# Kernel tuning notes

Hardware: AMD Instinct MI355X
Metric: run time of the kernel (lower is better)

## Reference

```python
import jax, jax.numpy as jnp
import numpy as np

B, S, HID, H, RELC = 2, 1024, 1024, 16, 64
D = HID // H          # head dim = 64
R = 2 * RELC + 1      # 129 relative-position buckets
NEG_INF = -10000.0
LN_EPS = 1e-12


def setup_inputs() -> dict:
    key = jax.random.key(0)
    ks = jax.random.split(key, 16)
    s = 0.02
    return {
        "query": jax.random.normal(ks[0], (B, S, HID), jnp.float32),
        "key": jax.random.normal(ks[1], (B, S, HID), jnp.float32),
        "value": jax.random.normal(ks[2], (B, S, HID), jnp.float32),
        "mask_k": jnp.ones((B, S), jnp.float32),
        "mask_qk": jnp.ones((B, S, S), jnp.float32),
        "rposi": jax.random.randint(ks[3], (B, S, S), 0, R, jnp.int32),
        "Wq": jax.random.normal(ks[4], (HID, HID), jnp.float32) * s,
        "bq": jnp.zeros((HID,), jnp.float32),
        "Wk": jax.random.normal(ks[5], (HID, HID), jnp.float32) * s,
        "bk": jnp.zeros((HID,), jnp.float32),
        "Wv": jax.random.normal(ks[6], (HID, HID), jnp.float32) * s,
        "bv": jnp.zeros((HID,), jnp.float32),
        "Wd": jax.random.normal(ks[7], (HID, HID), jnp.float32) * s,
        "bd": jnp.zeros((HID,), jnp.float32),
        "ln_g": jnp.ones((HID,), jnp.float32),
        "ln_b": jnp.zeros((HID,), jnp.float32),
        "edge_atts": jax.random.normal(ks[8], (R, D), jnp.float32) * s,
        "edge_values": jax.random.normal(ks[9], (R, D), jnp.float32) * s,
    }


def _heads(x):  # [B,S,HID] -> [B,H,S,D]
    return x.reshape(B, -1, H, D).transpose(0, 2, 1, 3)


def reference(query, key, value, mask_k, mask_qk, rposi,
              Wq, bq, Wk, bk, Wv, bv, Wd, bd, ln_g, ln_b,
              edge_atts, edge_values):
    q = _heads(query @ Wq + bq)   # [B,H,Q,D]
    k = _heads(key @ Wk + bk)     # [B,H,K,D]
    v = _heads(value @ Wv + bv)   # [B,H,K,D]

    rp = jnp.clip(rposi, -RELC, RELC) + RELC          # [B,Q,K] in [0,2*RELC]

    scores = jnp.einsum('bhqd,bhkd->bhqk', q, k)      # [B,H,Q,K]
    # relative-position attention bias: q . edge_atts[rp]
    q2 = jnp.einsum('bhqd,rd->bhqr', q, edge_atts)    # [B,H,Q,R]
    rscore = jnp.take_along_axis(
        q2, jnp.broadcast_to(rp[:, None], (B, H, S, S)), axis=-1)
    scores = (scores + rscore) / jnp.sqrt(jnp.float32(D))

    att_mask = mask_k[:, None, :] * mask_qk           # [B,Q,K]
    scores = scores + (1.0 - att_mask)[:, None] * NEG_INF
    probs = jax.nn.softmax(scores, axis=-1)           # [B,H,Q,K]

    ctx = jnp.einsum('bhqk,bhkd->bhqd', probs, v)     # [B,H,Q,D]
    rval = edge_values[rp]                            # [B,Q,K,D]
    ctx = ctx + jnp.einsum('bhqk,bqkd->bhqd', probs, rval)

    ctx = ctx.transpose(0, 2, 1, 3).reshape(B, S, HID)
    h = ctx @ Wd + bd
    x = h + query
    mu = jnp.mean(x, axis=-1, keepdims=True)
    var = jnp.mean(jnp.square(x - mu), axis=-1, keepdims=True)
    return (x - mu) * jax.lax.rsqrt(var + LN_EPS) * ln_g + ln_b
```

## Files before the change

kernel.cpp:

```cpp
#include <hip/hip_runtime.h>
#include <hip/hip_bf16.h>
#include <stdint.h>

#define B_    2
#define S_    1024
#define HID_  1024
#define H_    16
#define D_    64
#define R_    129
#define EST_  136
#define SENT_ 132
#define NTOK_ 2048
#define C2_   0.18033688011112042f

typedef __attribute__((ext_vector_type(8))) short bf16x8;
typedef __attribute__((ext_vector_type(4))) float f32x4;

__device__ __forceinline__ float bf2f(unsigned short s) {
  union { float f; unsigned int u; } v; v.u = ((unsigned int)s) << 16; return v.f;
}
__device__ __forceinline__ unsigned short f2bf(float f) {
  union { float f; unsigned int u; } v; v.f = f;
  return (unsigned short)((v.u + 0x7fff + ((v.u >> 16) & 1)) >> 16);
}

__global__ __launch_bounds__(256) void wt4_kernel(const float* __restrict__ Wq,
                                                  const float* __restrict__ Wk,
                                                  const float* __restrict__ Wv,
                                                  const float* __restrict__ Wd,
                                                  unsigned short* __restrict__ WqT,
                                                  unsigned short* __restrict__ WkT,
                                                  unsigned short* __restrict__ WvT,
                                                  unsigned short* __restrict__ WdT) {
  const float* W; unsigned short* Wt;
  switch (blockIdx.z) {
    case 0: W = Wq; Wt = WqT; break;
    case 1: W = Wk; Wt = WkT; break;
    case 2: W = Wv; Wt = WvT; break;
    default: W = Wd; Wt = WdT; break;
  }
  __shared__ float tile[32][33];
  const int n0 = blockIdx.x * 32, k0 = blockIdx.y * 32;
  const int tx = threadIdx.x, ty = threadIdx.y;
  #pragma unroll
  for (int i = 0; i < 32; i += 8)
    tile[ty + i][tx] = W[(size_t)(k0 + ty + i) * HID_ + n0 + tx];
  __syncthreads();
  #pragma unroll
  for (int i = 0; i < 32; i += 8)
    Wt[(size_t)(n0 + ty + i) * HID_ + k0 + tx] = f2bf(tile[tx][ty + i]);
}

__global__ __launch_bounds__(256) void evt_kernel(const float* __restrict__ EV,
                                                  unsigned short* __restrict__ EVt) {
  const int idx = blockIdx.x * 256 + threadIdx.x;
  if (idx < 64 * 160) {
    const int d = idx / 160, r = idx % 160;
    EVt[idx] = f2bf(r < R_ ? EV[(size_t)r * D_ + d] : 0.f);
  }
}

__global__ __launch_bounds__(256) void rpx_kernel(const int* __restrict__ rposi,
                                                  const float* __restrict__ mask_k,
                                                  const float* __restrict__ mask_qk,
                                                  unsigned char* __restrict__ rpx) {
  const int t = threadIdx.x;
  const int lo = t & 15, hi = (t >> 4) & 3, wq = (t >> 6) & 1, wk = (t >> 7) & 1;
  const int kt = blockIdx.x, q5 = blockIdx.y, b = blockIdx.z;
  unsigned char out[8];
  #pragma unroll
  for (int e = 0; e < 8; e++) {
    const int ct2 = e >> 2, j = e & 3;
    const int q = q5 * 32 + wq * 16 + hi * 4 + j;
    const int k = kt * 64 + wk * 32 + ct2 * 16 + lo;
    int rp = rposi[((size_t)b * S_ + q) * S_ + k];
    rp = min(max(rp, -64), 64) + 64;
    const float m = mask_qk[((size_t)b * S_ + q) * S_ + k] * mask_k[(size_t)b * S_ + k];
    out[e] = (m > 0.5f) ? (unsigned char)rp : (unsigned char)SENT_;
  }
  const size_t off = ((((((size_t)b * 32 + q5) * 16 + kt) * 2 + wk) * 2 + wq) * 4 + hi) * 16 + lo;
  *(uint2*)(rpx + off * 8) = *(uint2*)out;
}

__global__ __launch_bounds__(256) void qkv_gemm_kernel(
    const float* __restrict__ query, const float* __restrict__ key, const float* __restrict__ value,
    const unsigned short* __restrict__ WqT, const unsigned short* __restrict__ WkT,
    const unsigned short* __restrict__ WvT,
    const float* __restrict__ bq, const float* __restrict__ bk, const float* __restrict__ bvv,
    unsigned short* __restrict__ Qh, unsigned short* __restrict__ Kh, unsigned short* __restrict__ Vt) {
  const float* A; const unsigned short* Bt; const float* bias; unsigned short* Out; int omode;
  if (blockIdx.z == 0)      { A = query; Bt = WqT; bias = bq;  Out = Qh; omode = 0; }
  else if (blockIdx.z == 1) { A = key;   Bt = WkT; bias = bk;  Out = Kh; omode = 0; }
  else                      { A = value; Bt = WvT; bias = bvv; Out = Vt; omode = 1; }
  __shared__ __align__(16) unsigned short Alds[64][40];
  __shared__ __align__(16) unsigned short Blds[64][40];
  const int m0 = blockIdx.x * 64, n0 = blockIdx.y * 64;
  const int t = threadIdx.x;
  const int wave = t >> 6, lane = t & 63, lo = lane & 15, hi = lane >> 4;
  const int wr = wave >> 1, wc = wave & 1;
  const int row = t >> 2, col = (t & 3) * 8;
  const f32x4 zero4 = {0.f, 0.f, 0.f, 0.f};
  f32x4 acc[2][2] = {{zero4, zero4}, {zero4, zero4}};

  for (int k0 = 0; k0 < HID_; k0 += 32) {
    const float* asrc = A + (size_t)(m0 + row) * HID_ + k0 + col;
    f32x4 v0 = *(const f32x4*)asrc, v1 = *(const f32x4*)(asrc + 4);
    unsigned short ab[8];
    ab[0]=f2bf(v0.x); ab[1]=f2bf(v0.y); ab[2]=f2bf(v0.z); ab[3]=f2bf(v0.w);
    ab[4]=f2bf(v1.x); ab[5]=f2bf(v1.y); ab[6]=f2bf(v1.z); ab[7]=f2bf(v1.w);
    bf16x8 bb = *(const bf16x8*)(Bt + (size_t)(n0 + row) * HID_ + k0 + col);
    __syncthreads();
    *(bf16x8*)&Alds[row][col] = *(bf16x8*)ab;
    *(bf16x8*)&Blds[row][col] = bb;
    __syncthreads();
    bf16x8 af[2], bfr[2];
    #pragma unroll
    for (int a = 0; a < 2; a++) af[a]  = *(const bf16x8*)&Alds[wr*32 + a*16 + lo][hi*8];
    #pragma unroll
    for (int b2 = 0; b2 < 2; b2++) bfr[b2] = *(const bf16x8*)&Blds[wc*32 + b2*16 + lo][hi*8];
    #pragma unroll
    for (int a = 0; a < 2; a++)
      #pragma unroll
      for (int b2 = 0; b2 < 2; b2++)
        acc[a][b2] = __builtin_amdgcn_mfma_f32_16x16x32_bf16(af[a], bfr[b2], acc[a][b2], 0, 0, 0);
  }

  #pragma unroll
  for (int a = 0; a < 2; a++) {
    const int mg = m0 + wr*32 + a*16 + hi*4;
    #pragma unroll
    for (int b2 = 0; b2 < 2; b2++) {
      const int n = n0 + wc*32 + b2*16 + lo;
      const float bv = bias[n];
      const int hh = n >> 6, d = n & (D_ - 1);
      #pragma unroll
      for (int j = 0; j < 4; j++) {
        const float val = acc[a][b2][j] + bv;
        const int m = mg + j;
        const int bb = m >> 10, s = m & (S_ - 1);
        if (omode == 0)
          Out[(((size_t)(bb * H_ + hh)) * S_ + s) * D_ + d] = f2bf(val);
        else
          Out[(((size_t)(bb * H_ + hh)) * D_ + d) * S_ + s] = f2bf(val);
      }
    }
  }
}

__global__ __launch_bounds__(256) void d_gemm_kernel(const unsigned short* __restrict__ Actx,
                                                     const unsigned short* __restrict__ Bt,
                                                     const float* __restrict__ bias,
                                                     float* __restrict__ Out) {
  __shared__ __align__(16) unsigned short Alds[64][40];
  __shared__ __align__(16) unsigned short Blds[64][40];
  const int m0 = blockIdx.x * 64, n0 = blockIdx.y * 64;
  const int t = threadIdx.x;
  const int wave = t >> 6, lane = t & 63, lo = lane & 15, hi = lane >> 4;
  const int wr = wave >> 1, wc = wave & 1;
  const int row = t >> 2, col = (t & 3) * 8;
  const f32x4 zero4 = {0.f, 0.f, 0.f, 0.f};
  f32x4 acc[2][2] = {{zero4, zero4}, {zero4, zero4}};

  for (int k0 = 0; k0 < HID_; k0 += 32) {
    bf16x8 aa = *(const bf16x8*)(Actx + (size_t)(m0 + row) * HID_ + k0 + col);
    bf16x8 bb = *(const bf16x8*)(Bt + (size_t)(n0 + row) * HID_ + k0 + col);
    __syncthreads();
    *(bf16x8*)&Alds[row][col] = aa;
    *(bf16x8*)&Blds[row][col] = bb;
    __syncthreads();
    bf16x8 af[2], bfr[2];
    #pragma unroll
    for (int a = 0; a < 2; a++) af[a]  = *(const bf16x8*)&Alds[wr*32 + a*16 + lo][hi*8];
    #pragma unroll
    for (int b2 = 0; b2 < 2; b2++) bfr[b2] = *(const bf16x8*)&Blds[wc*32 + b2*16 + lo][hi*8];
    #pragma unroll
    for (int a = 0; a < 2; a++)
      #pragma unroll
      for (int b2 = 0; b2 < 2; b2++)
        acc[a][b2] = __builtin_amdgcn_mfma_f32_16x16x32_bf16(af[a], bfr[b2], acc[a][b2], 0, 0, 0);
  }

  #pragma unroll
  for (int a = 0; a < 2; a++) {
    const int mg = m0 + wr*32 + a*16 + hi*4;
    #pragma unroll
    for (int b2 = 0; b2 < 2; b2++) {
      const int n = n0 + wc*32 + b2*16 + lo;
      const float bv = bias[n];
      #pragma unroll
      for (int j = 0; j < 4; j++)
        Out[(size_t)(mg + j) * HID_ + n] = acc[a][b2][j] + bv;
    }
  }
}

__global__ __launch_bounds__(256) void eb_kernel(const unsigned short* __restrict__ Qh,
                                                 const float* __restrict__ EA,
                                                 unsigned short* __restrict__ Eb) {
  __shared__ __align__(16) unsigned short Qt[64][72];
  __shared__ __align__(16) unsigned short EAt[144][72];
  const int bh = blockIdx.y, s0 = blockIdx.x * 64;
  const int t = threadIdx.x, wave = t >> 6, lane = t & 63;
  const int lo = lane & 15, hi = lane >> 4;
  { const int row = t >> 2, c0 = (t & 3) * 16;
    const unsigned short* src = Qh + ((size_t)bh * S_ + s0 + row) * D_ + c0;
    *(bf16x8*)&Qt[row][c0]   = *(const bf16x8*)src;
    *(bf16x8*)&Qt[row][c0+8] = *(const bf16x8*)(src + 8); }
  for (int i = t; i < 144 * 64; i += 256) {
    const int r = i >> 6, d = i & 63;
    EAt[r][d] = f2bf(r < R_ ? EA[(size_t)r * D_ + d] : 0.f);
  }
  __syncthreads();
  bf16x8 af[2];
  af[0] = *(const bf16x8*)&Qt[wave*16 + lo][hi*8];
  af[1] = *(const bf16x8*)&Qt[wave*16 + lo][32 + hi*8];
  const f32x4 zero4 = {0.f, 0.f, 0.f, 0.f};
  f32x4 acc[9];
  #pragma unroll
  for (int rt = 0; rt < 9; rt++) acc[rt] = zero4;
  #pragma unroll
  for (int rt = 0; rt < 9; rt++)
    #pragma unroll
    for (int kk = 0; kk < 2; kk++) {
      bf16x8 bfr = *(const bf16x8*)&EAt[rt*16 + lo][kk*32 + hi*8];
      acc[rt] = __builtin_amdgcn_mfma_f32_16x16x32_bf16(af[kk], bfr, acc[rt], 0, 0, 0);
    }
  #pragma unroll
  for (int rt = 0; rt < 9; rt++) {
    const int r = rt * 16 + lo;
    if (r < EST_) {
      #pragma unroll
      for (int j = 0; j < 4; j++) {
        const int q = s0 + wave*16 + hi*4 + j;
        const float val = (r < R_) ? exp2f(acc[rt][j] * C2_) : 0.f;
        Eb[((size_t)bh * S_ + q) * EST_ + r] = f2bf(val);
      }
    }
  }
}


#define ABODY(KT, RX) do {                                                               \
    const int kw = (KT) * 64 + wk * 32;                                                  \
    int rpv[8];                                                                          \
    rpv[0] = (RX).x & 255;         rpv[1] = ((RX).x >> 8) & 255;                         \
    rpv[2] = ((RX).x >> 16) & 255; rpv[3] = (RX).x >> 24;                                \
    rpv[4] = (RX).y & 255;         rpv[5] = ((RX).y >> 8) & 255;                         \
    rpv[6] = ((RX).y >> 16) & 255; rpv[7] = (RX).y >> 24;                                \
    float ge[8];                                                                         \
    _Pragma("unroll")                                                                    \
    for (int e = 0; e < 8; e++)                                                          \
      ge[e] = bf2f(Uq.El[wq * 16 + hi * 4 + (e & 3)][rpv[e]]);                           \
    f32x4 sc0 = zero4, sc1 = zero4;                                                      \
    __builtin_amdgcn_s_setprio(1);                                                       \
    { bf16x8 kf0 = *(const bf16x8*)(Kbase + (size_t)(kw + lo) * D_ + hi * 8);            \
      bf16x8 kf1 = *(const bf16x8*)(Kbase + (size_t)(kw + lo) * D_ + 32 + hi * 8);       \
      bf16x8 kf2 = *(const bf16x8*)(Kbase + (size_t)(kw + 16 + lo) * D_ + hi * 8);       \
      bf16x8 kf3 = *(const bf16x8*)(Kbase + (size_t)(kw + 16 + lo) * D_ + 32 + hi * 8);  \
      sc0 = __builtin_amdgcn_mfma_f32_16x16x32_bf16(qfrag0, kf0, sc0, 0, 0, 0);          \
      sc0 = __builtin_amdgcn_mfma_f32_16x16x32_bf16(qfrag1, kf1, sc0, 0, 0, 0);          \
      sc1 = __builtin_amdgcn_mfma_f32_16x16x32_bf16(qfrag0, kf2, sc1, 0, 0, 0);          \
      sc1 = __builtin_amdgcn_mfma_f32_16x16x32_bf16(qfrag1, kf3, sc1, 0, 0, 0); }        \
    __builtin_amdgcn_s_setprio(0);                                                       \
    bf16x8 vf0 = *(const bf16x8*)(Vbase + (size_t)(lo) * S_ + kw + hi * 8);              \
    bf16x8 vf1 = *(const bf16x8*)(Vbase + (size_t)(16 + lo) * S_ + kw + hi * 8);         \
    bf16x8 vf2 = *(const bf16x8*)(Vbase + (size_t)(32 + lo) * S_ + kw + hi * 8);         \
    bf16x8 vf3 = *(const bf16x8*)(Vbase + (size_t)(48 + lo) * S_ + kw + hi * 8);         \
    _Pragma("unroll")                                                                    \
    for (int e = 0; e < 8; e++) {                                                        \
      const int j = e & 3;                                                               \
      const float sv = (e < 4) ? sc0[j] : sc1[j];                                        \
      const float p = exp2f(sv * C2_) * ge[e];                                           \
      lsum[j] += p;                                                                      \
      const int qr = wq * 16 + hi * 4 + j;                                               \
      if (rpv[e] == 128) r128[j] += p;                                                   \
      else atomicAdd(&hist[qr][rpv[e]], p);                                              \
      Plds[wave][hi * 4 + j][(e >> 2) * 16 + lo] = f2bf(p);                              \
    }                                                                                    \
    bf16x8 pf = *(const bf16x8*)&Plds[wave][lo][hi * 8];                                 \
    __builtin_amdgcn_s_setprio(1);                                                       \
    ctx[0] = __builtin_amdgcn_mfma_f32_16x16x32_bf16(pf, vf0, ctx[0], 0, 0, 0);          \
    ctx[1] = __builtin_amdgcn_mfma_f32_16x16x32_bf16(pf, vf1, ctx[1], 0, 0, 0);          \
    ctx[2] = __builtin_amdgcn_mfma_f32_16x16x32_bf16(pf, vf2, ctx[2], 0, 0, 0);          \
    ctx[3] = __builtin_amdgcn_mfma_f32_16x16x32_bf16(pf, vf3, ctx[3], 0, 0, 0);          \
    __builtin_amdgcn_s_setprio(0);                                                       \
  } while (0)

__global__ __launch_bounds__(256, 4) void attn_kernel(const unsigned short* __restrict__ Qh,
                                                      const unsigned short* __restrict__ Kh,
                                                      const unsigned short* __restrict__ Vt,
                                                      const unsigned short* __restrict__ Eb,
                                                      const unsigned char* __restrict__ rpx,
                                                      const unsigned short* __restrict__ EVt,
                                                      unsigned short* __restrict__ ctxb) {
  __shared__ union UU {
    unsigned short El[32][EST_];
    float red[2][16][65];
  } Uq;
  __shared__ float hist[32][EST_];
  __shared__ __align__(16) unsigned short Plds[4][16][40];
  __shared__ float lsumLDS[2][32];

  const int bh = blockIdx.y, b = bh >> 4, h = bh & 15;
  const int q5 = blockIdx.x, q0 = q5 * 32;
  const int t = threadIdx.x, wave = t >> 6, lane = t & 63;
  const int lo = lane & 15, hi = lane >> 4;
  const int wq = wave >> 1, wk = wave & 1;

  { const unsigned int* src = (const unsigned int*)(Eb + ((size_t)bh * S_ + q0) * EST_);
    unsigned int* dst = (unsigned int*)&Uq.El[0][0];
    for (int i = t; i < 32 * EST_ / 2; i += 256) dst[i] = src[i]; }
  for (int i = t; i < 32 * EST_; i += 256) (&hist[0][0])[i] = 0.f;

  bf16x8 qfrag0, qfrag1;
  { const unsigned short* qrow = Qh + ((size_t)bh * S_ + q0 + wq * 16 + lo) * D_;
    qfrag0 = *(const bf16x8*)(qrow + hi * 8);
    qfrag1 = *(const bf16x8*)(qrow + 32 + hi * 8); }

  const f32x4 zero4 = {0.f, 0.f, 0.f, 0.f};
  f32x4 ctx[4] = {zero4, zero4, zero4, zero4};
  float lsum[4] = {0.f, 0.f, 0.f, 0.f};
  float r128[4] = {0.f, 0.f, 0.f, 0.f};

  const unsigned short* Kbase = Kh + (size_t)bh * S_ * D_;
  const unsigned short* Vbase = Vt + (size_t)bh * D_ * S_;
  const unsigned char* RXp = rpx +
      (((((((size_t)b * 32 + q5) * 16) * 2 + wk) * 2 + wq) * 4 + hi) * 16 + lo) * 8;

  __syncthreads();

  uint2 rxA = *(const uint2*)(RXp);
  #pragma unroll 1
  for (int kt2 = 0; kt2 < 8; kt2++) {
    uint2 rxB = *(const uint2*)(RXp + (size_t)(2 * kt2 + 1) * 2048);
    ABODY(2 * kt2, rxA);
    if (kt2 < 7) rxA = *(const uint2*)(RXp + (size_t)(2 * kt2 + 2) * 2048);
    ABODY(2 * kt2 + 1, rxB);
  }

  #pragma unroll
  for (int j = 0; j < 4; j++) {
    float v = r128[j];
    v += __shfl_xor(v, 1); v += __shfl_xor(v, 2); v += __shfl_xor(v, 4); v += __shfl_xor(v, 8);
    if (lo == 0) atomicAdd(&hist[wq * 16 + hi * 4 + j][128], v);
    float w = lsum[j];
    w += __shfl_xor(w, 1); w += __shfl_xor(w, 2); w += __shfl_xor(w, 4); w += __shfl_xor(w, 8);
    if (lo == 0) lsumLDS[wk][wq * 16 + hi * 4 + j] = w;
  }
  __syncthreads();

  #pragma unroll
  for (int g2 = 0; g2 < 2; g2++) {
    const int r0 = (wk * 2 + g2) * 32;
    const float* hrow = &hist[wq * 16 + lo][r0 + hi * 8];
    bf16x8 hf;
    #pragma unroll
    for (int u = 0; u < 8; u++) hf[u] = (short)f2bf(hrow[u]);
    #pragma unroll
    for (int dt = 0; dt < 4; dt++) {
      bf16x8 ef = *(const bf16x8*)(EVt + (size_t)(dt * 16 + lo) * 160 + r0 + hi * 8);
      ctx[dt] = __builtin_amdgcn_mfma_f32_16x16x32_bf16(hf, ef, ctx[dt], 0, 0, 0);
    }
  }
  if (wk == 1) {
    #pragma unroll
    for (int dt = 0; dt < 4; dt++) {
      const float ev = bf2f(EVt[(size_t)(dt * 16 + lo) * 160 + 128]);
      #pragma unroll
      for (int j = 0; j < 4; j++) {
        ctx[dt][j] += hist[wq * 16 + hi * 4 + j][128] * ev;
        Uq.red[wq][hi * 4 + j][dt * 16 + lo] = ctx[dt][j];
      }
    }
  }
  __syncthreads();
  if (wk == 0) {
    float ls[4];
    #pragma unroll
    for (int j = 0; j < 4; j++)
      ls[j] = lsumLDS[0][wq * 16 + hi * 4 + j] + lsumLDS[1][wq * 16 + hi * 4 + j];
    #pragma unroll
    for (int dt = 0; dt < 4; dt++)
      #pragma unroll
      for (int j = 0; j < 4; j++) {
        const float val = (ctx[dt][j] + Uq.red[wq][hi * 4 + j][dt * 16 + lo]) / ls[j];
        const int q = q0 + wq * 16 + hi * 4 + j;
        ctxb[((size_t)b * S_ + q) * HID_ + h * D_ + dt * 16 + lo] = f2bf(val);
      }
  }
}

__global__ __launch_bounds__(256) void ln_kernel(const float* __restrict__ hbuf,
                                                 const float* __restrict__ query,
                                                 const float* __restrict__ g,
                                                 const float* __restrict__ bta,
                                                 float* __restrict__ out) {
  const int row = blockIdx.x, t = threadIdx.x;
  f32x4 hv = *(const f32x4*)(hbuf + (size_t)row * HID_ + t * 4);
  f32x4 qv = *(const f32x4*)(query + (size_t)row * HID_ + t * 4);
  f32x4 x;
  x.x = hv.x + qv.x; x.y = hv.y + qv.y; x.z = hv.z + qv.z; x.w = hv.w + qv.w;
  float s  = x.x + x.y + x.z + x.w;
  float s2 = x.x*x.x + x.y*x.y + x.z*x.z + x.w*x.w;
  #pragma unroll
  for (int m = 1; m < 64; m <<= 1) { s += __shfl_xor(s, m); s2 += __shfl_xor(s2, m); }
  __shared__ float w1[4], w2[4];
  const int wave = t >> 6;
  if ((t & 63) == 0) { w1[wave] = s; w2[wave] = s2; }
  __syncthreads();
  s  = w1[0] + w1[1] + w1[2] + w1[3];
  s2 = w2[0] + w2[1] + w2[2] + w2[3];
  const float mu  = s * (1.f / HID_);
  const float var = s2 * (1.f / HID_) - mu * mu;
  const float rstd = rsqrtf(var + 1e-12f);
  f32x4 gv = *(const f32x4*)(g + t * 4);
  f32x4 bv = *(const f32x4*)(bta + t * 4);
  f32x4 o;
  o.x = (x.x - mu) * rstd * gv.x + bv.x;
  o.y = (x.y - mu) * rstd * gv.y + bv.y;
  o.z = (x.z - mu) * rstd * gv.z + bv.z;
  o.w = (x.w - mu) * rstd * gv.w + bv.w;
  *(f32x4*)(out + (size_t)row * HID_ + t * 4) = o;
}

extern "C" void kernel_launch(void* const* d_in, const int* in_sizes, int n_in,
                              void* d_out, int out_size, void* d_ws, size_t ws_size,
                              hipStream_t stream) {
  const float* query   = (const float*)d_in[0];
  const float* key     = (const float*)d_in[1];
  const float* value   = (const float*)d_in[2];
  const float* mask_k  = (const float*)d_in[3];
  const float* mask_qk = (const float*)d_in[4];
  const int*   rposi   = (const int*)d_in[5];
  const float* Wq = (const float*)d_in[6];
  const float* bq = (const float*)d_in[7];
  const float* Wk = (const float*)d_in[8];
  const float* bk = (const float*)d_in[9];
  const float* Wv = (const float*)d_in[10];
  const float* bv = (const float*)d_in[11];
  const float* Wd = (const float*)d_in[12];
  const float* bd = (const float*)d_in[13];
  const float* ln_g = (const float*)d_in[14];
  const float* ln_b = (const float*)d_in[15];
  const float* edge_atts   = (const float*)d_in[16];
  const float* edge_values = (const float*)d_in[17];

  char* ws = (char*)d_ws;
  unsigned short* WqT  = (unsigned short*)(ws + 0);
  unsigned short* WkT  = (unsigned short*)(ws + 2097152);
  unsigned short* WvT  = (unsigned short*)(ws + 4194304);
  unsigned short* WdT  = (unsigned short*)(ws + 6291456);
  unsigned short* ctxb = (unsigned short*)(ws + 0);
  unsigned short* Qh   = (unsigned short*)(ws + 8388608);
  unsigned short* Kh   = (unsigned short*)(ws + 12582912);
  unsigned short* Vt   = (unsigned short*)(ws + 16777216);
  float*          hbuf = (float*)        (ws + 8388608);
  unsigned short* Eb   = (unsigned short*)(ws + 20971520);
  unsigned short* EVt  = (unsigned short*)(ws + 29884416);
  unsigned char*  rpx  = (unsigned char*) (ws + 29904896);

  wt4_kernel<<<dim3(32, 32, 4), dim3(32, 8), 0, stream>>>(Wq, Wk, Wv, Wd, WqT, WkT, WvT, WdT);
  evt_kernel<<<40, 256, 0, stream>>>(edge_values, EVt);
  rpx_kernel<<<dim3(16, 32, 2), 256, 0, stream>>>(rposi, mask_k, mask_qk, rpx);

  qkv_gemm_kernel<<<dim3(32, 16, 3), 256, 0, stream>>>(query, key, value, WqT, WkT, WvT,
                                                       bq, bk, bv, Qh, Kh, Vt);

  eb_kernel<<<dim3(S_/64, B_*H_), 256, 0, stream>>>(Qh, edge_atts, Eb);

  attn_kernel<<<dim3(S_/32, B_*H_), 256, 0, stream>>>(Qh, Kh, Vt, Eb, rpx, EVt, ctxb);

  d_gemm_kernel<<<dim3(32, 16), 256, 0, stream>>>(ctxb, WdT, bd, hbuf);

  ln_kernel<<<NTOK_, 256, 0, stream>>>(hbuf, query, ln_g, ln_b, (float*)d_out);
}
```

Baseline: 192.0 us.

## Use 128x128 GEMM tiles and defer relative-position histogram atomics past PV MFMA

The QKV and output-projection GEMMs now share a templated 128x128 tile body in which each wave computes 4x4 MFMA fragments. This raises data reuse per LDS load but leaves far fewer blocks: 384 for QKV and only 128 for the dense projection, which may underfill the GPU. In the attention kernel, the LDS atomic histogram updates and the r128 accumulation move to after the PV MFMAs, using bf16-rounded probabilities packed into registers, so the atomics can overlap the matrix work. That rounding slightly changes the numerics of the edge-value accumulation.

Result: slower. 209.4 us (+9.0%).

```diff
diff --git a/kernel.cpp b/kernel.cpp
--- a/kernel.cpp
+++ b/kernel.cpp
@@ -82,7 +82,86 @@
   *(uint2*)(rpx + off * 8) = *(uint2*)out;
 }
 
-__global__ __launch_bounds__(256) void qkv_gemm_kernel(
+template<int AMODE>
+__device__ __forceinline__ void gemm128_body(const void* __restrict__ Aptr,
+                                             const unsigned short* __restrict__ Bt,
+                                             const float* __restrict__ bias,
+                                             void* __restrict__ Out, int omode,
+                                             int m0, int n0) {
+  __shared__ __align__(16) unsigned short Alds[128][40];
+  __shared__ __align__(16) unsigned short Blds[128][40];
+  const int t = threadIdx.x;
+  const int wave = t >> 6, lane = t & 63, lo = lane & 15, hi = lane >> 4;
+  const int wr = wave >> 1, wc = wave & 1;
+  const int row = t >> 1, cb = (t & 1) * 16;
+  const f32x4 zero4 = {0.f, 0.f, 0.f, 0.f};
+  f32x4 acc[4][4];
+  #pragma unroll
+  for (int a = 0; a < 4; a++)
+    #pragma unroll
+    for (int b = 0; b < 4; b++) acc[a][b] = zero4;
+
+  for (int k0 = 0; k0 < HID_; k0 += 32) {
+    unsigned short abuf[16];
+    if (AMODE == 0) {
+      const float* s = (const float*)Aptr + (size_t)(m0 + row) * HID_ + k0 + cb;
+      f32x4 v0 = *(const f32x4*)s, v1 = *(const f32x4*)(s + 4);
+      f32x4 v2 = *(const f32x4*)(s + 8), v3 = *(const f32x4*)(s + 12);
+      abuf[0]=f2bf(v0.x); abuf[1]=f2bf(v0.y); abuf[2]=f2bf(v0.z); abuf[3]=f2bf(v0.w);
+      abuf[4]=f2bf(v1.x); abuf[5]=f2bf(v1.y); abuf[6]=f2bf(v1.z); abuf[7]=f2bf(v1.w);
+      abuf[8]=f2bf(v2.x); abuf[9]=f2bf(v2.y); abuf[10]=f2bf(v2.z); abuf[11]=f2bf(v2.w);
+      abuf[12]=f2bf(v3.x); abuf[13]=f2bf(v3.y); abuf[14]=f2bf(v3.z); abuf[15]=f2bf(v3.w);
+    } else {
+      const unsigned short* s = (const unsigned short*)Aptr + (size_t)(m0 + row) * HID_ + k0 + cb;
+      *(bf16x8*)&abuf[0] = *(const bf16x8*)s;
+      *(bf16x8*)&abuf[8] = *(const bf16x8*)(s + 8);
+    }
+    bf16x8 bb0 = *(const bf16x8*)(Bt + (size_t)(n0 + row) * HID_ + k0 + cb);
+    bf16x8 bb1 = *(const bf16x8*)(Bt + (size_t)(n0 + row) * HID_ + k0 + cb + 8);
+    __syncthreads();
+    *(bf16x8*)&Alds[row][cb]     = *(bf16x8*)&abuf[0];
+    *(bf16x8*)&Alds[row][cb + 8] = *(bf16x8*)&abuf[8];
+    *(bf16x8*)&Blds[row][cb]     = bb0;
+    *(bf16x8*)&Blds[row][cb + 8] = bb1;
+    __syncthreads();
+    bf16x8 af[4], bfr[4];
+    #pragma unroll
+    for (int a = 0; a < 4; a++) af[a]  = *(const bf16x8*)&Alds[wr*64 + a*16 + lo][hi*8];
+    #pragma unroll
+    for (int b = 0; b < 4; b++) bfr[b] = *(const bf16x8*)&Blds[wc*64 + b*16 + lo][hi*8];
+    #pragma unroll
+    for (int a = 0; a < 4; a++)
+      #pragma unroll
+      for (int b = 0; b < 4; b++)
+        acc[a][b] = __builtin_amdgcn_mfma_f32_16x16x32_bf16(af[a], bfr[b], acc[a][b], 0, 0, 0);
+  }
+
+  #pragma unroll
+  for (int a = 0; a < 4; a++) {
+    const int mg = m0 + wr*64 + a*16 + hi*4;
+    #pragma unroll
+    for (int b = 0; b < 4; b++) {
+      const int n = n0 + wc*64 + b*16 + lo;
+      const float bv = bias[n];
+      #pragma unroll
+      for (int j = 0; j < 4; j++) {
+        const float val = acc[a][b][j] + bv;
+        const int m = mg + j;
+        if (omode == 2) {
+          ((float*)Out)[(size_t)m * HID_ + n] = val;
+        } else {
+          const int bb = m >> 10, s = m & (S_ - 1), hh = n >> 6, d = n & (D_ - 1);
+          if (omode == 0)
+            ((unsigned short*)Out)[(((size_t)(bb * H_ + hh)) * S_ + s) * D_ + d] = f2bf(val);
+          else
+            ((unsigned short*)Out)[(((size_t)(bb * H_ + hh)) * D_ + d) * S_ + s] = f2bf(val);
+        }
+      }
+    }
+  }
+}
+
+__global__ __launch_bounds__(256) void qkv_gemm128_kernel(
     const float* __restrict__ query, const float* __restrict__ key, const float* __restrict__ value,
     const unsigned short* __restrict__ WqT, const unsigned short* __restrict__ WkT,
     const unsigned short* __restrict__ WvT,
@@ -92,106 +171,14 @@
   if (blockIdx.z == 0)      { A = query; Bt = WqT; bias = bq;  Out = Qh; omode = 0; }
   else if (blockIdx.z == 1) { A = key;   Bt = WkT; bias = bk;  Out = Kh; omode = 0; }
   else                      { A = value; Bt = WvT; bias = bvv; Out = Vt; omode = 1; }
-  __shared__ __align__(16) unsigned short Alds[64][40];
-  __shared__ __align__(16) unsigned short Blds[64][40];
-  const int m0 = blockIdx.x * 64, n0 = blockIdx.y * 64;
-  const int t = threadIdx.x;
-  const int wave = t >> 6, lane = t & 63, lo = lane & 15, hi = lane >> 4;
-  const int wr = wave >> 1, wc = wave & 1;
-  const int row = t >> 2, col = (t & 3) * 8;
-  const f32x4 zero4 = {0.f, 0.f, 0.f, 0.f};
-  f32x4 acc[2][2] = {{zero4, zero4}, {zero4, zero4}};
-
-  for (int k0 = 0; k0 < HID_; k0 += 32) {
-    const float* asrc = A + (size_t)(m0 + row) * HID_ + k0 + col;
-    f32x4 v0 = *(const f32x4*)asrc, v1 = *(const f32x4*)(asrc + 4);
-    unsigned short ab[8];
-    ab[0]=f2bf(v0.x); ab[1]=f2bf(v0.y); ab[2]=f2bf(v0.z); ab[3]=f2bf(v0.w);
-    ab[4]=f2bf(v1.x); ab[5]=f2bf(v1.y); ab[6]=f2bf(v1.z); ab[7]=f2bf(v1.w);
-    bf16x8 bb = *(const bf16x8*)(Bt + (size_t)(n0 + row) * HID_ + k0 + col);
-    __syncthreads();
-    *(bf16x8*)&Alds[row][col] = *(bf16x8*)ab;
-    *(bf16x8*)&Blds[row][col] = bb;
-    __syncthreads();
-    bf16x8 af[2], bfr[2];
-    #pragma unroll
-    for (int a = 0; a < 2; a++) af[a]  = *(const bf16x8*)&Alds[wr*32 + a*16 + lo][hi*8];
-    #pragma unroll
-    for (int b2 = 0; b2 < 2; b2++) bfr[b2] = *(const bf16x8*)&Blds[wc*32 + b2*16 + lo][hi*8];
-    #pragma unroll
-    for (int a = 0; a < 2; a++)
-      #pragma unroll
-      for (int b2 = 0; b2 < 2; b2++)
-        acc[a][b2] = __builtin_amdgcn_mfma_f32_16x16x32_bf16(af[a], bfr[b2], acc[a][b2], 0, 0, 0);
-  }
-
-  #pragma unroll
-  for (int a = 0; a < 2; a++) {
-    const int mg = m0 + wr*32 + a*16 + hi*4;
-    #pragma unroll
-    for (int b2 = 0; b2 < 2; b2++) {
-      const int n = n0 + wc*32 + b2*16 + lo;
-      const float bv = bias[n];
-      const int hh = n >> 6, d = n & (D_ - 1);
-      #pragma unroll
-      for (int j = 0; j < 4; j++) {
-        const float val = acc[a][b2][j] + bv;
-        const int m = mg + j;
-        const int bb = m >> 10, s = m & (S_ - 1);
-        if (omode == 0)
-          Out[(((size_t)(bb * H_ + hh)) * S_ + s) * D_ + d] = f2bf(val);
-        else
-          Out[(((size_t)(bb * H_ + hh)) * D_ + d) * S_ + s] = f2bf(val);
-      }
-    }
-  }
-}
-
-__global__ __launch_bounds__(256) void d_gemm_kernel(const unsigned short* __restrict__ Actx,
-                                                     const unsigned short* __restrict__ Bt,
-                                                     const float* __restrict__ bias,
-                                                     float* __restrict__ Out) {
-  __shared__ __align__(16) unsigned short Alds[64][40];
-  __shared__ __align__(16) unsigned short Blds[64][40];
-  const int m0 = blockIdx.x * 64, n0 = blockIdx.y * 64;
-  const int t = threadIdx.x;
-  const int wave = t >> 6, lane = t & 63, lo = lane & 15, hi = lane >> 4;
-  const int wr = wave >> 1, wc = wave & 1;
-  const int row = t >> 2, col = (t & 3) * 8;
-  const f32x4 zero4 = {0.f, 0.f, 0.f, 0.f};
-  f32x4 acc[2][2] = {{zero4, zero4}, {zero4, zero4}};
-
-  for (int k0 = 0; k0 < HID_; k0 += 32) {
-    bf16x8 aa = *(const bf16x8*)(Actx + (size_t)(m0 + row) * HID_ + k0 + col);
-    bf16x8 bb = *(const bf16x8*)(Bt + (size_t)(n0 + row) * HID_ + k0 + col);
-    __syncthreads();
-    *(bf16x8*)&Alds[row][col] = aa;
-    *(bf16x8*)&Blds[row][col] = bb;
-    __syncthreads();
-    bf16x8 af[2], bfr[2];
-    #pragma unroll
-    for (int a = 0; a < 2; a++) af[a]  = *(const bf16x8*)&Alds[wr*32 + a*16 + lo][hi*8];
-    #pragma unroll
-    for (int b2 = 0; b2 < 2; b2++) bfr[b2] = *(const bf16x8*)&Blds[wc*32 + b2*16 + lo][hi*8];
-    #pragma unroll
-    for (int a = 0; a < 2; a++)
-      #pragma unroll
-      for (int b2 = 0; b2 < 2; b2++)
-        acc[a][b2] = __builtin_amdgcn_mfma_f32_16x16x32_bf16(af[a], bfr[b2], acc[a][b2], 0, 0, 0);
-  }
-
-  #pragma unroll
-  for (int a = 0; a < 2; a++) {
-    const int mg = m0 + wr*32 + a*16 + hi*4;
-    #pragma unroll
-    for (int b2 = 0; b2 < 2; b2++) {
-      const int n = n0 + wc*32 + b2*16 + lo;
-      const float bv = bias[n];
-      #pragma unroll
-      for (int j = 0; j < 4; j++)
-        Out[(size_t)(mg + j) * HID_ + n] = acc[a][b2][j] + bv;
-    }
-  }
+  gemm128_body<0>(A, Bt, bias, Out, omode, blockIdx.x * 128, blockIdx.y * 128);
+}
+
+__global__ __launch_bounds__(256) void d_gemm128_kernel(const unsigned short* __restrict__ Actx,
+                                                        const unsigned short* __restrict__ Bt,
+                                                        const float* __restrict__ bias,
+                                                        float* __restrict__ Out) {
+  gemm128_body<1>(Actx, Bt, bias, Out, 2, blockIdx.x * 128, blockIdx.y * 128);
 }
 
 __global__ __launch_bounds__(256) void eb_kernel(const unsigned short* __restrict__ Qh,
@@ -242,15 +229,12 @@
 
 #define ABODY(KT, RX) do {                                                               \
     const int kw = (KT) * 64 + wk * 32;                                                  \
-    int rpv[8];                                                                          \
-    rpv[0] = (RX).x & 255;         rpv[1] = ((RX).x >> 8) & 255;                         \
-    rpv[2] = ((RX).x >> 16) & 255; rpv[3] = (RX).x >> 24;                                \
-    rpv[4] = (RX).y & 255;         rpv[5] = ((RX).y >> 8) & 255;                         \
-    rpv[6] = ((RX).y >> 16) & 255; rpv[7] = (RX).y >> 24;                                \
     float ge[8];                                                                         \
     _Pragma("unroll")                                                                    \
-    for (int e = 0; e < 8; e++)                                                          \
-      ge[e] = bf2f(Uq.El[wq * 16 + hi * 4 + (e & 3)][rpv[e]]);                           \
+    for (int e = 0; e < 8; e++) {                                                        \
+      const int rp = (int)(((e < 4 ? (RX).x : (RX).y) >> ((e & 3) * 8)) & 255u);         \
+      ge[e] = bf2f(Uq.El[wq * 16 + hi * 4 + (e & 3)][rp]);                               \
+    }                                                                                    \
     f32x4 sc0 = zero4, sc1 = zero4;                                                      \
     __builtin_amdgcn_s_setprio(1);                                                       \
     { bf16x8 kf0 = *(const bf16x8*)(Kbase + (size_t)(kw + lo) * D_ + hi * 8);            \
@@ -266,16 +250,19 @@
     bf16x8 vf1 = *(const bf16x8*)(Vbase + (size_t)(16 + lo) * S_ + kw + hi * 8);         \
     bf16x8 vf2 = *(const bf16x8*)(Vbase + (size_t)(32 + lo) * S_ + kw + hi * 8);         \
     bf16x8 vf3 = *(const bf16x8*)(Vbase + (size_t)(48 + lo) * S_ + kw + hi * 8);         \
+    unsigned int pvp0, pvp1, pvp2, pvp3;                                                 \
     _Pragma("unroll")                                                                    \
     for (int e = 0; e < 8; e++) {                                                        \
       const int j = e & 3;                                                               \
       const float sv = (e < 4) ? sc0[j] : sc1[j];                                        \
       const float p = exp2f(sv * C2_) * ge[e];                                           \
       lsum[j] += p;                                                                      \
-      const int qr = wq * 16 + hi * 4 + j;                                               \
-      if (rpv[e] == 128) r128[j] += p;                                                   \
-      else atomicAdd(&hist[qr][rpv[e]], p);                                              \
-      Plds[wave][hi * 4 + j][(e >> 2) * 16 + lo] = f2bf(p);                              \
+      const unsigned int pb = f2bf(p);                                                   \
+      if (e == 0) pvp0 = pb;       else if (e == 1) pvp0 |= pb << 16;                    \
+      else if (e == 2) pvp1 = pb;  else if (e == 3) pvp1 |= pb << 16;                    \
+      else if (e == 4) pvp2 = pb;  else if (e == 5) pvp2 |= pb << 16;                    \
+      else if (e == 6) pvp3 = pb;  else              pvp3 |= pb << 16;                   \
+      Plds[wave][hi * 4 + j][(e >> 2) * 16 + lo] = (unsigned short)pb;                   \
     }                                                                                    \
     bf16x8 pf = *(const bf16x8*)&Plds[wave][lo][hi * 8];                                 \
     __builtin_amdgcn_s_setprio(1);                                                       \
@@ -284,6 +271,14 @@
     ctx[2] = __builtin_amdgcn_mfma_f32_16x16x32_bf16(pf, vf2, ctx[2], 0, 0, 0);          \
     ctx[3] = __builtin_amdgcn_mfma_f32_16x16x32_bf16(pf, vf3, ctx[3], 0, 0, 0);          \
     __builtin_amdgcn_s_setprio(0);                                                       \
+    _Pragma("unroll")                                                                    \
+    for (int e = 0; e < 8; e++) {                                                        \
+      const int rp = (int)(((e < 4 ? (RX).x : (RX).y) >> ((e & 3) * 8)) & 255u);         \
+      const unsigned int pw = (e < 2) ? pvp0 : (e < 4) ? pvp1 : (e < 6) ? pvp2 : pvp3;   \
+      const float pr = bf2f((unsigned short)((pw >> ((e & 1) * 16)) & 0xFFFFu));         \
+      if (rp == 128) r128[e & 3] += pr;                                                  \
+      else atomicAdd(&hist[wq * 16 + hi * 4 + (e & 3)][rp], pr);                         \
+    }                                                                                    \
   } while (0)
 
 __global__ __launch_bounds__(256, 4) void attn_kernel(const unsigned short* __restrict__ Qh,
@@ -463,14 +458,14 @@
   evt_kernel<<<40, 256, 0, stream>>>(edge_values, EVt);
   rpx_kernel<<<dim3(16, 32, 2), 256, 0, stream>>>(rposi, mask_k, mask_qk, rpx);
 
-  qkv_gemm_kernel<<<dim3(32, 16, 3), 256, 0, stream>>>(query, key, value, WqT, WkT, WvT,
-                                                       bq, bk, bv, Qh, Kh, Vt);
+  qkv_gemm128_kernel<<<dim3(16, 8, 3), 256, 0, stream>>>(query, key, value, WqT, WkT, WvT,
+                                                         bq, bk, bv, Qh, Kh, Vt);
 
   eb_kernel<<<dim3(S_/64, B_*H_), 256, 0, stream>>>(Qh, edge_atts, Eb);
 
   attn_kernel<<<dim3(S_/32, B_*H_), 256, 0, stream>>>(Qh, Kh, Vt, Eb, rpx, EVt, ctxb);
 
-  d_gemm_kernel<<<dim3(32, 16), 256, 0, stream>>>(ctxb, WdT, bd, hbuf);
+  d_gemm128_kernel<<<dim3(16, 8), 256, 0, stream>>>(ctxb, WdT, bd, hbuf);
 
   ln_kernel<<<NTOK_, 256, 0, stream>>>(hbuf, query, ln_g, ln_b, (float*)d_out);
 }
```

## Hoist K/V loads, defer histogram atomics past PV MFMA, remap attention block order

Applied to the files above, without the earlier changes.

The attention loop body now issues all K and V fragment loads before the QK MFMAs and moves the LDS histogram atomics after the PV MFMAs, using packed bf16 probabilities kept in registers. The goal is to overlap global load latency and LDS atomic traffic with matrix work instead of serializing them. The launch also becomes a 1D grid with a swizzled mapping that groups 8 heads per query tile, presumably to improve L2 locality of rpx/mask data across heads. The histogram now accumulates bf16-rounded probabilities, a small precision change, and more values stay live in registers.

Result: no change. 190.0 us (-1.0%).

```diff
diff --git a/kernel.cpp b/kernel.cpp
--- a/kernel.cpp
+++ b/kernel.cpp
@@ -242,40 +242,40 @@
 
 #define ABODY(KT, RX) do {                                                               \
     const int kw = (KT) * 64 + wk * 32;                                                  \
-    int rpv[8];                                                                          \
-    rpv[0] = (RX).x & 255;         rpv[1] = ((RX).x >> 8) & 255;                         \
-    rpv[2] = ((RX).x >> 16) & 255; rpv[3] = (RX).x >> 24;                                \
-    rpv[4] = (RX).y & 255;         rpv[5] = ((RX).y >> 8) & 255;                         \
-    rpv[6] = ((RX).y >> 16) & 255; rpv[7] = (RX).y >> 24;                                \
     float ge[8];                                                                         \
     _Pragma("unroll")                                                                    \
-    for (int e = 0; e < 8; e++)                                                          \
-      ge[e] = bf2f(Uq.El[wq * 16 + hi * 4 + (e & 3)][rpv[e]]);                           \
-    f32x4 sc0 = zero4, sc1 = zero4;                                                      \
-    __builtin_amdgcn_s_setprio(1);                                                       \
-    { bf16x8 kf0 = *(const bf16x8*)(Kbase + (size_t)(kw + lo) * D_ + hi * 8);            \
-      bf16x8 kf1 = *(const bf16x8*)(Kbase + (size_t)(kw + lo) * D_ + 32 + hi * 8);       \
-      bf16x8 kf2 = *(const bf16x8*)(Kbase + (size_t)(kw + 16 + lo) * D_ + hi * 8);       \
-      bf16x8 kf3 = *(const bf16x8*)(Kbase + (size_t)(kw + 16 + lo) * D_ + 32 + hi * 8);  \
-      sc0 = __builtin_amdgcn_mfma_f32_16x16x32_bf16(qfrag0, kf0, sc0, 0, 0, 0);          \
-      sc0 = __builtin_amdgcn_mfma_f32_16x16x32_bf16(qfrag1, kf1, sc0, 0, 0, 0);          \
-      sc1 = __builtin_amdgcn_mfma_f32_16x16x32_bf16(qfrag0, kf2, sc1, 0, 0, 0);          \
-      sc1 = __builtin_amdgcn_mfma_f32_16x16x32_bf16(qfrag1, kf3, sc1, 0, 0, 0); }        \
-    __builtin_amdgcn_s_setprio(0);                                                       \
+    for (int e = 0; e < 8; e++) {                                                        \
+      const int rp = (int)(((e < 4 ? (RX).x : (RX).y) >> ((e & 3) * 8)) & 255u);         \
+      ge[e] = bf2f(Uq.El[wq * 16 + hi * 4 + (e & 3)][rp]);                               \
+    }                                                                                    \
+    bf16x8 kf0 = *(const bf16x8*)(Kbase + (size_t)(kw + lo) * D_ + hi * 8);              \
+    bf16x8 kf1 = *(const bf16x8*)(Kbase + (size_t)(kw + lo) * D_ + 32 + hi * 8);         \
+    bf16x8 kf2 = *(const bf16x8*)(Kbase + (size_t)(kw + 16 + lo) * D_ + hi * 8);         \
+    bf16x8 kf3 = *(const bf16x8*)(Kbase + (size_t)(kw + 16 + lo) * D_ + 32 + hi * 8);    \
     bf16x8 vf0 = *(const bf16x8*)(Vbase + (size_t)(lo) * S_ + kw + hi * 8);              \
     bf16x8 vf1 = *(const bf16x8*)(Vbase + (size_t)(16 + lo) * S_ + kw + hi * 8);         \
     bf16x8 vf2 = *(const bf16x8*)(Vbase + (size_t)(32 + lo) * S_ + kw + hi * 8);         \
     bf16x8 vf3 = *(const bf16x8*)(Vbase + (size_t)(48 + lo) * S_ + kw + hi * 8);         \
+    f32x4 sc0 = zero4, sc1 = zero4;                                                      \
+    __builtin_amdgcn_s_setprio(1);                                                       \
+    sc0 = __builtin_amdgcn_mfma_f32_16x16x32_bf16(qfrag0, kf0, sc0, 0, 0, 0);            \
+    sc0 = __builtin_amdgcn_mfma_f32_16x16x32_bf16(qfrag1, kf1, sc0, 0, 0, 0);            \
+    sc1 = __builtin_amdgcn_mfma_f32_16x16x32_bf16(qfrag0, kf2, sc1, 0, 0, 0);            \
+    sc1 = __builtin_amdgcn_mfma_f32_16x16x32_bf16(qfrag1, kf3, sc1, 0, 0, 0);            \
+    __builtin_amdgcn_s_setprio(0);                                                       \
+    unsigned int pvp0, pvp1, pvp2, pvp3;                                                 \
     _Pragma("unroll")                                                                    \
     for (int e = 0; e < 8; e++) {                                                        \
       const int j = e & 3;                                                               \
       const float sv = (e < 4) ? sc0[j] : sc1[j];                                        \
       const float p = exp2f(sv * C2_) * ge[e];                                           \
       lsum[j] += p;                                                                      \
-      const int qr = wq * 16 + hi * 4 + j;                                               \
-      if (rpv[e] == 128) r128[j] += p;                                                   \
-      else atomicAdd(&hist[qr][rpv[e]], p);                                              \
-      Plds[wave][hi * 4 + j][(e >> 2) * 16 + lo] = f2bf(p);                              \
+      const unsigned int pb = f2bf(p);                                                   \
+      if (e == 0) pvp0 = pb;       else if (e == 1) pvp0 |= pb << 16;                    \
+      else if (e == 2) pvp1 = pb;  else if (e == 3) pvp1 |= pb << 16;                    \
+      else if (e == 4) pvp2 = pb;  else if (e == 5) pvp2 |= pb << 16;                    \
+      else if (e == 6) pvp3 = pb;  else              pvp3 |= pb << 16;                   \
+      Plds[wave][hi * 4 + j][(e >> 2) * 16 + lo] = (unsigned short)pb;                   \
     }                                                                                    \
     bf16x8 pf = *(const bf16x8*)&Plds[wave][lo][hi * 8];                                 \
     __builtin_amdgcn_s_setprio(1);                                                       \
@@ -284,6 +284,14 @@
     ctx[2] = __builtin_amdgcn_mfma_f32_16x16x32_bf16(pf, vf2, ctx[2], 0, 0, 0);          \
     ctx[3] = __builtin_amdgcn_mfma_f32_16x16x32_bf16(pf, vf3, ctx[3], 0, 0, 0);          \
     __builtin_amdgcn_s_setprio(0);                                                       \
+    _Pragma("unroll")                                                                    \
+    for (int e = 0; e < 8; e++) {                                                        \
+      const int rp = (int)(((e < 4 ? (RX).x : (RX).y) >> ((e & 3) * 8)) & 255u);         \
+      const unsigned int pw = (e < 2) ? pvp0 : (e < 4) ? pvp1 : (e < 6) ? pvp2 : pvp3;   \
+      const float pr = bf2f((unsigned short)((pw >> ((e & 1) * 16)) & 0xFFFFu));         \
+      if (rp == 128) r128[e & 3] += pr;                                                  \
+      else atomicAdd(&hist[wq * 16 + hi * 4 + (e & 3)][rp], pr);                         \
+    }                                                                                    \
   } while (0)
 
 __global__ __launch_bounds__(256, 4) void attn_kernel(const unsigned short* __restrict__ Qh,
@@ -301,8 +309,11 @@
   __shared__ __align__(16) unsigned short Plds[4][16][40];
   __shared__ float lsumLDS[2][32];
 
-  const int bh = blockIdx.y, b = bh >> 4, h = bh & 15;
-  const int q5 = blockIdx.x, q0 = q5 * 32;
+  const int lin = blockIdx.x;
+  const int bh = (lin & 7) + 8 * (lin >> 8);
+  const int q5 = (lin >> 3) & 31;
+  const int b = bh >> 4, h = bh & 15;
+  const int q0 = q5 * 32;
   const int t = threadIdx.x, wave = t >> 6, lane = t & 63;
   const int lo = lane & 15, hi = lane >> 4;
   const int wq = wave >> 1, wk = wave & 1;
@@ -468,7 +479,7 @@
 
   eb_kernel<<<dim3(S_/64, B_*H_), 256, 0, stream>>>(Qh, edge_atts, Eb);
 
-  attn_kernel<<<dim3(S_/32, B_*H_), 256, 0, stream>>>(Qh, Kh, Vt, Eb, rpx, EVt, ctxb);
+  attn_kernel<<<1024, 256, 0, stream>>>(Qh, Kh, Vt, Eb, rpx, EVt, ctxb);
 
   d_gemm_kernel<<<dim3(32, 16), 256, 0, stream>>>(ctxb, WdT, bd, hbuf);
 
```
